# Kernel tuning notes

Measured on AMD Instinct MI355X. Metric: run time of the kernel, lower is better.

Reference implementation:

```python
import jax, jax.numpy as jnp
import numpy as np

N_PROP = 1024; C_FEAT = 32
ROI = 7; SR = 6; S = ROI * SR
NMS_THR = 0.01; NMS_K = 100
X_MIN, Z_MAX, VOX = -40.0, 70.0, 0.1

_SIGNS = np.array([[sx, sy, sz] for sx in (-1, 1) for sy in (-1, 1) for sz in (-1, 1)], np.float32)


def project_to_bev(a):
    # anchors [N,6] = (x,y,z,dx,dy,dz); BEV pixel box (x right, z forward->down)
    x, z, dx, dz = a[:, 0], a[:, 2], a[:, 3], a[:, 5]
    return jnp.stack([(x - dx * 0.5 - X_MIN) / VOX,
                      (Z_MAX - (z + dz * 0.5)) / VOX,
                      (x + dx * 0.5 - X_MIN) / VOX,
                      (Z_MAX - (z - dz * 0.5)) / VOX], axis=1)


def project_to_img(a, P, image_shape):
    # axis-aligned 3D box -> 8 corners -> project with P [3,4] -> min/max, clip
    corners = a[:, None, :3] + _SIGNS[None] * (a[:, None, 3:6] * 0.5)  # [N,8,3]
    hom = jnp.concatenate([corners, jnp.ones_like(corners[..., :1])], -1)
    proj = jnp.einsum('nkj,ij->nki', hom, P)
    z = jnp.maximum(proj[..., 2], 0.1)
    u, v = proj[..., 0] / z, proj[..., 1] / z
    H = image_shape[0].astype(u.dtype); W = image_shape[1].astype(u.dtype)
    return jnp.stack([jnp.clip(u.min(1), 0., W), jnp.clip(v.min(1), 0., H),
                      jnp.clip(u.max(1), 0., W), jnp.clip(v.max(1), 0., H)], 1)


def roi_align(feat, boxes):
    # feat [C,H,W], boxes [N,4] xyxy; aligned=True, sampling_ratio=SR, scale=1.0
    C, H, W = feat.shape
    grid = (jnp.arange(S, dtype=feat.dtype) + 0.5) / S

    def one(box):
        x1, y1, x2, y2 = box[0] - 0.5, box[1] - 0.5, box[2] - 0.5, box[3] - 0.5
        xs = x1 + grid * (x2 - x1)
        ys = y1 + grid * (y2 - y1)
        x0 = jnp.clip(jnp.floor(xs), 0, W - 1); y0 = jnp.clip(jnp.floor(ys), 0, H - 1)
        wx = jnp.clip(xs - x0, 0., 1.); wy = jnp.clip(ys - y0, 0., 1.)
        x0i = x0.astype(jnp.int32); y0i = y0.astype(jnp.int32)
        x1i = jnp.minimum(x0i + 1, W - 1); y1i = jnp.minimum(y0i + 1, H - 1)
        g = lambda yi, xi: feat[:, yi[:, None], xi[None, :]]  # [C,S,S]
        val = (g(y0i, x0i) * ((1 - wy)[:, None] * (1 - wx)[None, :])
             + g(y0i, x1i) * ((1 - wy)[:, None] * wx[None, :])
             + g(y1i, x0i) * (wy[:, None] * (1 - wx)[None, :])
             + g(y1i, x1i) * (wy[:, None] * wx[None, :]))
        return val.reshape(C, ROI, SR, ROI, SR).mean(axis=(2, 4))

    return jax.vmap(one)(boxes)  # [N,C,7,7]


def nms(boxes, scores, thr, k):
    areas = (boxes[:, 2] - boxes[:, 0]) * (boxes[:, 3] - boxes[:, 1])

    def step(s, _):
        i = jnp.argmax(s)
        b = boxes[i]
        xx1 = jnp.maximum(boxes[:, 0], b[0]); yy1 = jnp.maximum(boxes[:, 1], b[1])
        xx2 = jnp.minimum(boxes[:, 2], b[2]); yy2 = jnp.minimum(boxes[:, 3], b[3])
        inter = jnp.maximum(xx2 - xx1, 0.) * jnp.maximum(yy2 - yy1, 0.)
        iou = inter / (areas + areas[i] - inter + 1e-6)
        s = jnp.where(iou > thr, -jnp.inf, s).at[i].set(-jnp.inf)
        return s, i

    _, idx = jax.lax.scan(step, scores, None, length=k)
    return idx


def setup_inputs() -> dict:
    key = jax.random.key(0)
    ks = jax.random.split(key, 8)
    u = jax.random.uniform(ks[0], (N_PROP, 6))
    x = u[:, 0] * 70. - 35.; y = u[:, 1] * 2. - 1.; z = u[:, 2] * 60. + 5.
    dims = u[:, 3:6] * 3. + 1.
    top_anchors = jnp.concatenate([jnp.stack([x, y, z], 1), dims], 1)
    f = 721.5377
    calib = jnp.array([[f, 0., 609.56, 44.857],
                       [0., f, 172.854, 0.2163],
                       [0., 0., 1., 0.00275]], jnp.float32)
    D = C_FEAT * ROI * ROI
    w = lambda k, shp: jax.random.normal(k, shp, jnp.float32) * 0.02
    return {
        'img_feat_map': jax.random.normal(ks[1], (1, C_FEAT, 360, 1200), jnp.float32),
        'bev_feat_map': jax.random.normal(ks[2], (1, C_FEAT, 700, 800), jnp.float32),
        'top_anchors': top_anchors, 'calib': calib,
        'ground_plane': jnp.array([0., -1., 0., 1.65], jnp.float32),
        'img_mask': jnp.ones((1, 1, 1, 1), jnp.float32),
        'bev_mask': jnp.ones((1, 1, 1, 1), jnp.float32),
        'W1': w(ks[3], (D, 2048)), 'b1': jnp.zeros((2048,), jnp.float32),
        'W2': w(ks[4], (2048, 2048)), 'b2': jnp.zeros((2048,), jnp.float32),
        'Wc': w(ks[5], (2048, 2)), 'bc': jnp.zeros((2,), jnp.float32),
        'Wo': w(ks[6], (2048, 10)), 'bo': jnp.zeros((10,), jnp.float32),
        'Wa': w(ks[7], (2048, 2)), 'ba': jnp.zeros((2,), jnp.float32),
        'image_shape': jnp.array([360, 1200], jnp.int32),
    }


def reference(img_feat_map, bev_feat_map, top_anchors, calib, ground_plane,
              img_mask, bev_mask, W1, b1, W2, b2, Wc, bc, Wo, bo, Wa, ba, image_shape):
    bev_boxes = project_to_bev(top_anchors)
    img_boxes = project_to_img(top_anchors, calib, image_shape)
    rois_rgb = roi_align((img_mask * img_feat_map)[0], img_boxes)
    rois_bev = roi_align((bev_mask * bev_feat_map)[0], bev_boxes)
    fused = (rois_rgb + rois_bev) / (img_mask + bev_mask)[0, 0, 0, 0]  # mean fusion
    h = fused.reshape(fused.shape[0], -1)
    h = jax.nn.relu(h @ W1 + b1)
    h = jax.nn.relu(h @ W2 + b2)
    obj = h @ Wc + bc    # [N,2]
    off = h @ Wo + bo    # [N,10]
    ang = h @ Wa + ba    # [N,2]
    obj_soft = jax.nn.softmax(obj, axis=1)
    orient = jnp.arctan2(ang[:, 1], ang[:, 0])
    pred_anchors = top_anchors + off[:, :6] + 0.0 * ground_plane.sum()
    pred_box = jnp.concatenate([pred_anchors, jnp.zeros_like(pred_anchors[:, :1])], 1)
    pred_bev = project_to_bev(pred_anchors)
    top_scores = obj[:, 1:].max(axis=1)  # max over fg classes
    idx = nms(pred_bev, top_scores, NMS_THR, NMS_K)
    return (obj_soft[idx], pred_anchors[idx], off[idx], pred_box[idx], orient[idx])
```

## Files before the change

### kernel.cpp

```cpp
#include <hip/hip_runtime.h>
#include <math.h>

#define N_PROP 1024
#define C_FEAT 32
#define ROI 7
#define SR 6
#define S_GRID 42
#define IMG_H 360
#define IMG_W 1200
#define BEV_H 700
#define BEV_W 800
#define D_FEAT (C_FEAT*ROI*ROI)
#define HID 2048
#define NMS_K 100
#define NMS_THR 0.01f

typedef __attribute__((ext_vector_type(8))) short bf16x8;
typedef __attribute__((ext_vector_type(4))) float f32x4;
typedef __attribute__((ext_vector_type(2), aligned(4))) float f32x2u;
typedef __attribute__((ext_vector_type(4), aligned(4))) float f32x4u;

#define WS_IMG_BOXES 0
#define WS_BEV_BOXES (WS_IMG_BOXES + 4*N_PROP)
#define WS_OBJS      (WS_BEV_BOXES + 4*N_PROP)
#define WS_OFF       (WS_OBJS + 2*N_PROP)
#define WS_ORIENT    (WS_OFF + 10*N_PROP)
#define WS_PRED      (WS_ORIENT + N_PROP)
#define WS_PBEV      (WS_PRED + 6*N_PROP)
#define WS_SCORES    (WS_PBEV + 4*N_PROP)
#define WS_IDX       (WS_SCORES + N_PROP)
#define WS_SORT      (WS_IDX + 128)
#define WS_R0        40960
#define WS_R1        (WS_R0 + N_PROP*D_FEAT)
#define WS_IMGT      WS_R1
#define WS_FUSED_HI  (WS_R0 + 2*N_PROP*D_FEAT)
#define WS_FUSED_LO  (WS_FUSED_HI + N_PROP*D_FEAT/2)
#define WS_H1HI      WS_R0
#define WS_H1LO      (WS_R0 + N_PROP*HID/2)
#define WS_H2        (WS_R0 + N_PROP*HID)
#define WS_NMSM      WS_R0

__device__ __forceinline__ unsigned int bf16_rtn(float x) {
    unsigned int u = __float_as_uint(x);
    return (u + 0x7FFFu + ((u >> 16) & 1u)) >> 16;
}

__global__ void boxes_kernel(const float* __restrict__ anchors,
                             const float* __restrict__ calib,
                             const int* __restrict__ imshape,
                             float* __restrict__ img_boxes,
                             float* __restrict__ bev_boxes) {
    int n = blockIdx.x * blockDim.x + threadIdx.x;
    if (n >= N_PROP) return;
    float x = anchors[n*6+0], y = anchors[n*6+1], z = anchors[n*6+2];
    float dx = anchors[n*6+3], dy = anchors[n*6+4], dz = anchors[n*6+5];

    bev_boxes[n*4+0] = ((x - dx*0.5f) - (-40.0f)) / 0.1f;
    bev_boxes[n*4+1] = (70.0f - (z + dz*0.5f)) / 0.1f;
    bev_boxes[n*4+2] = ((x + dx*0.5f) - (-40.0f)) / 0.1f;
    bev_boxes[n*4+3] = (70.0f - (z - dz*0.5f)) / 0.1f;

    float P[12];
    #pragma unroll
    for (int i = 0; i < 12; i++) P[i] = calib[i];

    float umin = 1e30f, vmin = 1e30f, umax = -1e30f, vmax = -1e30f;
    #pragma unroll
    for (int k = 0; k < 8; k++) {
        float fsx = (k & 4) ? 1.0f : -1.0f;
        float fsy = (k & 2) ? 1.0f : -1.0f;
        float fsz = (k & 1) ? 1.0f : -1.0f;
        float cx = x + fsx * dx * 0.5f;
        float cy = y + fsy * dy * 0.5f;
        float cz = z + fsz * dz * 0.5f;
        float p0 = P[0]*cx + P[1]*cy + P[2]*cz + P[3];
        float p1 = P[4]*cx + P[5]*cy + P[6]*cz + P[7];
        float p2 = P[8]*cx + P[9]*cy + P[10]*cz + P[11];
        float zz = fmaxf(p2, 0.1f);
        float u = p0 / zz, v = p1 / zz;
        umin = fminf(umin, u); umax = fmaxf(umax, u);
        vmin = fminf(vmin, v); vmax = fmaxf(vmax, v);
    }
    float Hf = (float)imshape[0];
    float Wf = (float)imshape[1];
    img_boxes[n*4+0] = fminf(fmaxf(umin, 0.0f), Wf);
    img_boxes[n*4+1] = fminf(fmaxf(vmin, 0.0f), Hf);
    img_boxes[n*4+2] = fminf(fmaxf(umax, 0.0f), Wf);
    img_boxes[n*4+3] = fminf(fmaxf(vmax, 0.0f), Hf);
}

__global__ __launch_bounds__(256) void transpose_img_kernel(
        const float* __restrict__ in, float* __restrict__ out, int c0) {
    __shared__ float lds[64*9];
    int y = blockIdx.y;
    int x0 = blockIdx.x * 64;
    int xl = threadIdx.x & 63;
    int ch = threadIdx.x >> 6;
    int x = x0 + xl;
    #pragma unroll
    for (int i = 0; i < 2; i++) {
        int c = ch + i*4;
        float v = 0.0f;
        if (x < IMG_W)
            v = in[(size_t)(c0+c)*IMG_H*IMG_W + (size_t)y*IMG_W + x];
        lds[xl*9 + c] = v;
    }
    __syncthreads();
    int c8 = threadIdx.x & 7;
    int xp = threadIdx.x >> 3;
    #pragma unroll
    for (int j = 0; j < 2; j++) {
        int xx = x0 + xp + j*32;
        if (xx < IMG_W)
            out[((size_t)y*IMG_W + xx)*8 + c8] = lds[(xp + j*32)*9 + c8];
    }
}

__global__ __launch_bounds__(256) void roi_img_cl_kernel(
        const float* __restrict__ T, const float* __restrict__ img_boxes,
        float* __restrict__ img_out, int c0) {
    int b = blockIdx.x;
    __shared__ float s_xw[S_GRID], s_yw[S_GRID];
    __shared__ int   s_xi[S_GRID], s_yr[S_GRID];
    __shared__ float s_out[8*49];
    int tid = threadIdx.x;
    if (tid < S_GRID) {
        float g = ((float)tid + 0.5f) / (float)S_GRID;
        float bx1 = img_boxes[b*4+0] - 0.5f, by1 = img_boxes[b*4+1] - 0.5f;
        float bx2 = img_boxes[b*4+2] - 0.5f, by2 = img_boxes[b*4+3] - 0.5f;
        float xs = bx1 + g * (bx2 - bx1);
        float x0f = fminf(fmaxf(floorf(xs), 0.0f), (float)(IMG_W-2));
        s_xw[tid] = fminf(fmaxf(xs - x0f, 0.0f), 1.0f);
        s_xi[tid] = (int)x0f * 8;
        float ys = by1 + g * (by2 - by1);
        float y0f = fminf(fmaxf(floorf(ys), 0.0f), (float)(IMG_H-2));
        s_yw[tid] = fminf(fmaxf(ys - y0f, 0.0f), 1.0f);
        s_yr[tid] = (int)y0f * (IMG_W*8);
    }
    __syncthreads();

    int wv   = tid >> 6;
    int lane = tid & 63;
    int sy2 = lane >> 5;
    int sxb = (lane >> 4) & 1;
    int px  = (lane >> 1) & 7;
    int c4  = lane & 1;
    bool act = (px < 7);

    for (int pyi = 0; pyi < 2; pyi++) {
        int py = wv + pyi*4;
        if (py > 6) break;
        f32x4 acc = {0.f, 0.f, 0.f, 0.f};
        if (act) {
            #pragma unroll
            for (int t = 0; t < 3; t++) {
                int sy = py*6 + t*2 + sy2;
                int row0 = s_yr[sy];
                float wy = s_yw[sy];
                #pragma unroll
                for (int s = 0; s < 3; s++) {
                    int sx = px*6 + s*2 + sxb;
                    int col = s_xi[sx] + c4*4;
                    const float* p00 = T + row0 + col;
                    f32x4 v00 = *(const f32x4*)(p00);
                    f32x4 v01 = *(const f32x4*)(p00 + 8);
                    f32x4 v10 = *(const f32x4*)(p00 + IMG_W*8);
                    f32x4 v11 = *(const f32x4*)(p00 + IMG_W*8 + 8);
                    float wx = s_xw[sx];
                    #pragma unroll
                    for (int e = 0; e < 4; e++) {
                        float top = fmaf(wx, v01[e] - v00[e], v00[e]);
                        float bot = fmaf(wx, v11[e] - v10[e], v10[e]);
                        acc[e] += fmaf(wy, bot - top, top);
                    }
                }
            }
        }
        #pragma unroll
        for (int e = 0; e < 4; e++) acc[e] += __shfl_xor(acc[e], 32);
        #pragma unroll
        for (int e = 0; e < 4; e++) acc[e] += __shfl_xor(acc[e], 16);
        if (act && sy2 == 0 && sxb == 0) {
            #pragma unroll
            for (int e = 0; e < 4; e++)
                s_out[(c4*4+e)*49 + py*7 + px] = acc[e];
        }
    }
    __syncthreads();
    float* op = img_out + (size_t)b * D_FEAT + c0*49;
    for (int t = tid; t < 8*49; t += 256) op[t] = s_out[t];
}

__global__ __launch_bounds__(64, 8) void roi_bev_kernel(
        const float* __restrict__ bevF, const float* __restrict__ bev_boxes,
        float* __restrict__ bev_out) {
    int gx = blockIdx.x;
    int b  = blockIdx.y;
    int c0 = gx * 3;
    int nch = (C_FEAT - c0 < 3) ? (C_FEAT - c0) : 3;
    const int W = BEV_W, H = BEV_H;

    int lane = threadIdx.x;
    __shared__ int   s_xi[S_GRID];
    __shared__ float s_xw[S_GRID];
    __shared__ int   s_row0[S_GRID];
    __shared__ float s_wy[S_GRID];

    if (lane < S_GRID) {
        float g = ((float)lane + 0.5f) / (float)S_GRID;
        float bx1 = bev_boxes[b*4+0], by1 = bev_boxes[b*4+1];
        float bx2 = bev_boxes[b*4+2], by2 = bev_boxes[b*4+3];
        float e1 = bx1 - 0.5f, e2 = bx2 - 0.5f;
        float xs = e1 + g * (e2 - e1);
        float x0f = fminf(fmaxf(floorf(xs), 0.0f), (float)(W-2));
        s_xw[lane] = fminf(fmaxf(xs - x0f, 0.0f), 1.0f);
        s_xi[lane] = (int)x0f;
        float d1 = by1 - 0.5f, d2 = by2 - 0.5f;
        float ys = d1 + g * (d2 - d1);
        float y0f = fminf(fmaxf(floorf(ys), 0.0f), (float)(H-2));
        s_wy[lane] = fminf(fmaxf(ys - y0f, 0.0f), 1.0f);
        s_row0[lane] = (int)y0f * W;
    }
    __syncthreads();

    int gl = lane / 21;
    int j  = lane - gl*21;
    bool act = (gl < nch);

    int basecol = 0;
    float wa0=0.f,wa1=0.f,wa2=0.f,wa3=0.f;
    float wb0=0.f,wb1=0.f,wb2=0.f,wb3=0.f;
    if (act) {
        int x0a = s_xi[2*j];
        int x0b = s_xi[2*j+1];
        float wxa = s_xw[2*j], wxb = s_xw[2*j+1];
        basecol = min(x0a, W-4);
        int ca = x0a - basecol;
        int cb = min(x0b - basecol, 2);
        wa0 = (ca==0)? 1.f-wxa : 0.f;
        wa1 = (ca==0)? wxa : ((ca==1)? 1.f-wxa : 0.f);
        wa2 = (ca==1)? wxa : ((ca==2)? 1.f-wxa : 0.f);
        wa3 = (ca==2)? wxa : 0.f;
        wb0 = (cb==0)? 1.f-wxb : 0.f;
        wb1 = (cb==0)? wxb : ((cb==1)? 1.f-wxb : 0.f);
        wb2 = (cb==1)? wxb : ((cb==2)? 1.f-wxb : 0.f);
        wb3 = (cb==2)? wxb : 0.f;
    }
    const float* fp = bevF + (size_t)(c0 + (act ? gl : 0)) * W * H + basecol;
    int pxw = j / 3;
    bool wr = act && (j - pxw*3 == 0);
    float* op = bev_out + (size_t)b * D_FEAT + (c0+gl)*49;

    #pragma unroll 1
    for (int py = 0; py < ROI; py++) {
        float pl = 0.0f;
        #pragma unroll
        for (int sy = 0; sy < SR; sy++) {
            int yi = py*SR + sy;
            int r0 = s_row0[yi];
            float wy = s_wy[yi];
            if (act) {
                f32x4u q0 = *(const f32x4u*)(fp + r0);
                f32x4u q1 = *(const f32x4u*)(fp + r0 + W);
                float tA = fmaf(q0.x,wa0, fmaf(q0.y,wa1, fmaf(q0.z,wa2, q0.w*wa3)));
                float bA = fmaf(q1.x,wa0, fmaf(q1.y,wa1, fmaf(q1.z,wa2, q1.w*wa3)));
                float tB = fmaf(q0.x,wb0, fmaf(q0.y,wb1, fmaf(q0.z,wb2, q0.w*wb3)));
                float bB = fmaf(q1.x,wb0, fmaf(q1.y,wb1, fmaf(q1.z,wb2, q1.w*wb3)));
                pl += fmaf(wy, bA - tA, tA);
                pl += fmaf(wy, bB - tB, tB);
            }
        }
        float s = pl + __shfl_down(pl, 1) + __shfl_down(pl, 2);
        if (wr) op[py*ROI + pxw] = s;
    }
}

__global__ __launch_bounds__(256) void combine_split_kernel(
        const float4* __restrict__ img, const float4* __restrict__ bev,
        const float* __restrict__ img_mask, const float* __restrict__ bev_mask,
        ushort4* __restrict__ outHi, ushort4* __restrict__ outLo, int total4) {
    int i = blockIdx.x * 256 + threadIdx.x;
    if (i >= total4) return;
    float m0 = img_mask[0], m1 = bev_mask[0];
    float inv = 1.0f / ((m0 + m1) * 36.0f);
    float w0 = m0 * inv, w1 = m1 * inv;
    float4 a = img[i], b = bev[i];
    float v[4] = { w0*a.x + w1*b.x, w0*a.y + w1*b.y, w0*a.z + w1*b.z, w0*a.w + w1*b.w };
    ushort4 hv, lv;
    unsigned short* hp = &hv.x;
    unsigned short* lp = &lv.x;
    #pragma unroll
    for (int e = 0; e < 4; e++) {
        unsigned int rh = bf16_rtn(v[e]);
        float lo = v[e] - __uint_as_float(rh << 16);
        hp[e] = (unsigned short)rh;
        lp[e] = (unsigned short)bf16_rtn(lo);
    }
    outHi[i] = hv;
    outLo[i] = lv;
}

#define LDK 40
template<int EPI>
__global__ __launch_bounds__(256) void gemm_bf16x2_kernel(
        const unsigned short* __restrict__ Ahi, const unsigned short* __restrict__ Alo,
        const float* __restrict__ W, const float* __restrict__ bias, int K,
        unsigned short* __restrict__ outHi, unsigned short* __restrict__ outLo,
        float* __restrict__ outF) {
    __shared__ short AsH[64*LDK], AsL[64*LDK];
    __shared__ short BsH[128*LDK], BsL[128*LDK];

    const int tid = threadIdx.x;
    const int m0 = blockIdx.y * 64, n0 = blockIdx.x * 128;

    const int am = tid >> 2, ac = tid & 3;
    const uint4* ApH = (const uint4*)(Ahi + (size_t)(m0 + am) * K + ac*8);
    const uint4* ApL = (const uint4*)(Alo + (size_t)(m0 + am) * K + ac*8);
    const int nn = tid & 127, rbase = (tid >> 7) * 16;
    const float* Bp = W + (size_t)rbase * 2048 + n0 + nn;

    const int lane = tid & 63, wave = tid >> 6;
    const int wm = wave & 1, wn = wave >> 1;
    const int l15 = lane & 15, quad = lane >> 4;

    f32x4 acc[2][4];
    #pragma unroll
    for (int i = 0; i < 2; i++)
        #pragma unroll
        for (int j = 0; j < 4; j++)
            acc[i][j] = (f32x4){0.f, 0.f, 0.f, 0.f};

    const int nK = K >> 5;
    uint4 aHr = ApH[0];
    uint4 aLr = ApL[0];
    float bReg[16];
    #pragma unroll
    for (int j = 0; j < 16; j++) bReg[j] = Bp[(size_t)j * 2048];

    for (int ks = 0; ks < nK; ks++) {
        __syncthreads();
        *(uint4*)&AsH[am*LDK + ac*8] = aHr;
        *(uint4*)&AsL[am*LDK + ac*8] = aLr;
        {
            unsigned short hv[16], lv[16];
            #pragma unroll
            for (int j = 0; j < 16; j++) {
                unsigned int rh = bf16_rtn(bReg[j]);
                float lo = bReg[j] - __uint_as_float(rh << 16);
                hv[j] = (unsigned short)rh;
                lv[j] = (unsigned short)bf16_rtn(lo);
            }
            *(uint4*)&BsH[nn*LDK + rbase + 0] = *(uint4*)&hv[0];
            *(uint4*)&BsH[nn*LDK + rbase + 8] = *(uint4*)&hv[8];
            *(uint4*)&BsL[nn*LDK + rbase + 0] = *(uint4*)&lv[0];
            *(uint4*)&BsL[nn*LDK + rbase + 8] = *(uint4*)&lv[8];
        }
        __syncthreads();
        if (ks + 1 < nK) {
            int k0n = (ks + 1) * 32;
            aHr = ApH[k0n >> 3];
            aLr = ApL[k0n >> 3];
            #pragma unroll
            for (int j = 0; j < 16; j++) bReg[j] = Bp[(size_t)(k0n + j) * 2048];
        }
        const short* aBH = AsH + (wm*32 + l15)*LDK + quad*8;
        const short* aBL = AsL + (wm*32 + l15)*LDK + quad*8;
        const short* bBH = BsH + (wn*64 + l15)*LDK + quad*8;
        const short* bBL = BsL + (wn*64 + l15)*LDK + quad*8;
        bf16x8 aH0 = *(const bf16x8*)(aBH);
        bf16x8 aH1 = *(const bf16x8*)(aBH + 16*LDK);
        bf16x8 aL0 = *(const bf16x8*)(aBL);
        bf16x8 aL1 = *(const bf16x8*)(aBL + 16*LDK);
        #pragma unroll
        for (int nt = 0; nt < 4; nt++) {
            bf16x8 bH = *(const bf16x8*)(bBH + nt*16*LDK);
            bf16x8 bL = *(const bf16x8*)(bBL + nt*16*LDK);
            acc[0][nt] = __builtin_amdgcn_mfma_f32_16x16x32_bf16(aH0, bH, acc[0][nt], 0, 0, 0);
            acc[0][nt] = __builtin_amdgcn_mfma_f32_16x16x32_bf16(aH0, bL, acc[0][nt], 0, 0, 0);
            acc[0][nt] = __builtin_amdgcn_mfma_f32_16x16x32_bf16(aL0, bH, acc[0][nt], 0, 0, 0);
            acc[1][nt] = __builtin_amdgcn_mfma_f32_16x16x32_bf16(aH1, bH, acc[1][nt], 0, 0, 0);
            acc[1][nt] = __builtin_amdgcn_mfma_f32_16x16x32_bf16(aH1, bL, acc[1][nt], 0, 0, 0);
            acc[1][nt] = __builtin_amdgcn_mfma_f32_16x16x32_bf16(aL1, bH, acc[1][nt], 0, 0, 0);
        }
    }

    #pragma unroll
    for (int mt = 0; mt < 2; mt++) {
        #pragma unroll
        for (int nt = 0; nt < 4; nt++) {
            int n = n0 + wn*64 + nt*16 + l15;
            float bv = bias[n];
            #pragma unroll
            for (int reg = 0; reg < 4; reg++) {
                int m = m0 + wm*32 + mt*16 + quad*4 + reg;
                float v = fmaxf(acc[mt][nt][reg] + bv, 0.0f);
                if (EPI == 1) {
                    unsigned int rh = bf16_rtn(v);
                    float lo = v - __uint_as_float(rh << 16);
                    outHi[(size_t)m * 2048 + n] = (unsigned short)rh;
                    outLo[(size_t)m * 2048 + n] = (unsigned short)bf16_rtn(lo);
                } else {
                    outF[(size_t)m * 2048 + n] = v;
                }
            }
        }
    }
}

__global__ __launch_bounds__(256) void heads_kernel(
        const float* __restrict__ h,
        const float* __restrict__ Wc, const float* __restrict__ bc,
        const float* __restrict__ Wo, const float* __restrict__ bo,
        const float* __restrict__ Wa, const float* __restrict__ ba,
        const float* __restrict__ anchors,
        float* __restrict__ obj_soft, float* __restrict__ off_out,
        float* __restrict__ orient, float* __restrict__ pred,
        float* __restrict__ pbev, float* __restrict__ scores) {
    int row = blockIdx.x;
    const float* hr = h + (size_t)row * HID;
    float acc[14];
    #pragma unroll
    for (int j = 0; j < 14; j++) acc[j] = 0.0f;
    for (int k = threadIdx.x; k < HID; k += 256) {
        float hv = hr[k];
        acc[0]  += hv * Wc[k*2+0];
        acc[1]  += hv * Wc[k*2+1];
        #pragma unroll
        for (int j = 0; j < 10; j++) acc[2+j] += hv * Wo[k*10+j];
        acc[12] += hv * Wa[k*2+0];
        acc[13] += hv * Wa[k*2+1];
    }
    #pragma unroll
    for (int d = 32; d > 0; d >>= 1) {
        #pragma unroll
        for (int j = 0; j < 14; j++) acc[j] += __shfl_down(acc[j], d);
    }
    __shared__ float red[4][14];
    int wid = threadIdx.x >> 6, lane = threadIdx.x & 63;
    if (lane == 0) {
        #pragma unroll
        for (int j = 0; j < 14; j++) red[wid][j] = acc[j];
    }
    __syncthreads();
    if (threadIdx.x == 0) {
        float f[14];
        #pragma unroll
        for (int j = 0; j < 14; j++)
            f[j] = red[0][j] + red[1][j] + red[2][j] + red[3][j];
        float obj0 = f[0] + bc[0], obj1 = f[1] + bc[1];
        float offv[10];
        #pragma unroll
        for (int j = 0; j < 10; j++) offv[j] = f[2+j] + bo[j];
        float ang0 = f[12] + ba[0], ang1 = f[13] + ba[1];
        float mx = fmaxf(obj0, obj1);
        float e0 = expf(obj0 - mx), e1 = expf(obj1 - mx);
        float den = e0 + e1;
        obj_soft[row*2+0] = e0 / den;
        obj_soft[row*2+1] = e1 / den;
        scores[row] = obj1;
        orient[row] = atan2f(ang1, ang0);
        float pa[6];
        #pragma unroll
        for (int j = 0; j < 6; j++) {
            pa[j] = anchors[row*6+j] + offv[j];
            pred[row*6+j] = pa[j];
        }
        #pragma unroll
        for (int j = 0; j < 10; j++) off_out[row*10+j] = offv[j];
        float x = pa[0], z = pa[2], ddx = pa[3], ddz = pa[5];
        pbev[row*4+0] = ((x - ddx*0.5f) - (-40.0f)) / 0.1f;
        pbev[row*4+1] = (70.0f - (z + ddz*0.5f)) / 0.1f;
        pbev[row*4+2] = ((x + ddx*0.5f) - (-40.0f)) / 0.1f;
        pbev[row*4+3] = (70.0f - (z - ddz*0.5f)) / 0.1f;
    }
}

__global__ __launch_bounds__(256) void nms_mask_kernel(
        const float* __restrict__ boxes, unsigned long long* __restrict__ M) {
    int i = blockIdx.x;
    const float4* bp = (const float4*)boxes;
    float4 bi4 = bp[i];
    float ai = (bi4.z - bi4.x) * (bi4.w - bi4.y);
    int lane = threadIdx.x & 63, wave = threadIdx.x >> 6;
    #pragma unroll
    for (int it = 0; it < 4; it++) {
        int q = it*256 + wave*64 + lane;
        float4 bq = bp[q];
        float aq = (bq.z - bq.x) * (bq.w - bq.y);
        float xx1 = fmaxf(bi4.x, bq.x), yy1 = fmaxf(bi4.y, bq.y);
        float xx2 = fminf(bi4.z, bq.z), yy2 = fminf(bi4.w, bq.w);
        float inter = fmaxf(xx2 - xx1, 0.0f) * fmaxf(yy2 - yy1, 0.0f);
        float iou = inter / (ai + aq - inter + 1e-6f);
        unsigned long long bal = __ballot(iou > NMS_THR);
        if (lane == 0) M[(size_t)i*16 + it*4 + wave] = bal;
    }
}

__global__ __launch_bounds__(256) void nms_rank_kernel(
        const float* __restrict__ scores, int* __restrict__ sorted) {
    int i = blockIdx.x;
    unsigned int u = __float_as_uint(scores[i]);
    unsigned int ki = (u & 0x80000000u) ? ~u : (u | 0x80000000u);
    unsigned long long keyi = ((unsigned long long)ki << 10) | (unsigned)(1023 - i);
    int cnt = 0;
    #pragma unroll
    for (int t = 0; t < 4; t++) {
        int j = threadIdx.x + t*256;
        unsigned int uj = __float_as_uint(scores[j]);
        unsigned int kj = (uj & 0x80000000u) ? ~uj : (uj | 0x80000000u);
        unsigned long long keyj = ((unsigned long long)kj << 10) | (unsigned)(1023 - j);
        cnt += (keyj > keyi) ? 1 : 0;
    }
    #pragma unroll
    for (int d = 32; d > 0; d >>= 1) cnt += __shfl_down(cnt, d);
    __shared__ int red[4];
    if ((threadIdx.x & 63) == 0) red[threadIdx.x >> 6] = cnt;
    __syncthreads();
    if (threadIdx.x == 0) sorted[red[0] + red[1] + red[2] + red[3]] = i;
}

__global__ void nms_scan2_kernel(const int* __restrict__ sorted,
                                 const unsigned long long* __restrict__ M,
                                 int* __restrict__ idx_out) {
    int lane = threadIdx.x;
    unsigned long long sup = 0ull;
    int n = 0;
    for (int chunk = 0; chunk < 16 && n < NMS_K; chunk++) {
        int cid = sorted[chunk*64 + lane];
        int cw = cid >> 6, cb = cid & 63;
        unsigned long long supw = __shfl(sup, cw);
        unsigned long long mask = __ballot(((supw >> cb) & 1ull) == 0ull);
        while (mask != 0ull && n < NMS_K) {
            int p = __ffsll(mask) - 1;
            int c = __shfl(cid, p);
            if (lane == 0) idx_out[n] = c;
            n++;
            unsigned long long roww = (lane < 16) ? M[(size_t)c*16 + lane] : 0ull;
            sup |= roww;
            unsigned long long tw = __shfl(roww, cw);
            unsigned long long kill = __ballot(((tw >> cb) & 1ull) != 0ull);
            mask &= ~kill;
            mask &= ~(1ull << p);
        }
    }
    if (lane == 0) {
        for (; n < NMS_K; n++) idx_out[n] = 0;
    }
}

__global__ void gather_kernel(const int* __restrict__ idx,
                              const float* __restrict__ obj_soft,
                              const float* __restrict__ pred,
                              const float* __restrict__ off,
                              const float* __restrict__ orient,
                              float* __restrict__ out) {
    int i = threadIdx.x;
    if (i < NMS_K) {
        int j = idx[i];
        out[2*i+0] = obj_soft[j*2+0];
        out[2*i+1] = obj_soft[j*2+1];
        #pragma unroll
        for (int t = 0; t < 6; t++) out[200 + 6*i + t] = pred[j*6+t];
        #pragma unroll
        for (int t = 0; t < 10; t++) out[800 + 10*i + t] = off[j*10+t];
        #pragma unroll
        for (int t = 0; t < 6; t++) out[1800 + 7*i + t] = pred[j*6+t];
        out[1800 + 7*i + 6] = 0.0f;
        out[2500 + i] = orient[j];
    }
}

extern "C" void kernel_launch(void* const* d_in, const int* in_sizes, int n_in,
                              void* d_out, int out_size, void* d_ws, size_t ws_size,
                              hipStream_t stream) {
    const float* imgF     = (const float*)d_in[0];
    const float* bevF     = (const float*)d_in[1];
    const float* anchors  = (const float*)d_in[2];
    const float* calib    = (const float*)d_in[3];
    const float* img_mask = (const float*)d_in[5];
    const float* bev_mask = (const float*)d_in[6];
    const float* W1 = (const float*)d_in[7];
    const float* b1 = (const float*)d_in[8];
    const float* W2 = (const float*)d_in[9];
    const float* b2 = (const float*)d_in[10];
    const float* Wc = (const float*)d_in[11];
    const float* bc = (const float*)d_in[12];
    const float* Wo = (const float*)d_in[13];
    const float* bo = (const float*)d_in[14];
    const float* Wa = (const float*)d_in[15];
    const float* ba = (const float*)d_in[16];
    const int* image_shape = (const int*)d_in[17];

    float* ws = (float*)d_ws;
    float* img_boxes = ws + WS_IMG_BOXES;
    float* bev_boxes = ws + WS_BEV_BOXES;
    float* obj_soft  = ws + WS_OBJS;
    float* off       = ws + WS_OFF;
    float* orient    = ws + WS_ORIENT;
    float* pred      = ws + WS_PRED;
    float* pbev      = ws + WS_PBEV;
    float* scores    = ws + WS_SCORES;
    int*   idx       = (int*)(ws + WS_IDX);
    int*   sorted    = (int*)(ws + WS_SORT);
    float* img_s     = ws + WS_R0;
    float* bev_s     = ws + WS_R1;
    float* img_t     = ws + WS_IMGT;
    unsigned short* fusedHi = (unsigned short*)(ws + WS_FUSED_HI);
    unsigned short* fusedLo = (unsigned short*)(ws + WS_FUSED_LO);
    unsigned short* h1Hi    = (unsigned short*)(ws + WS_H1HI);
    unsigned short* h1Lo    = (unsigned short*)(ws + WS_H1LO);
    float* h2        = ws + WS_H2;
    unsigned long long* nmsM = (unsigned long long*)(ws + WS_NMSM);

    boxes_kernel<<<N_PROP/64, 64, 0, stream>>>(anchors, calib, image_shape,
                                               img_boxes, bev_boxes);
    for (int ch = 0; ch < 4; ch++) {
        transpose_img_kernel<<<dim3((IMG_W+63)/64, IMG_H), 256, 0, stream>>>(
            imgF, img_t, ch*8);
        roi_img_cl_kernel<<<N_PROP, 256, 0, stream>>>(
            img_t, img_boxes, img_s, ch*8);
    }
    roi_bev_kernel<<<dim3(11, N_PROP), 64, 0, stream>>>(
        bevF, bev_boxes, bev_s);
    combine_split_kernel<<<(N_PROP*D_FEAT/4 + 255)/256, 256, 0, stream>>>(
        (const float4*)img_s, (const float4*)bev_s, img_mask, bev_mask,
        (ushort4*)fusedHi, (ushort4*)fusedLo, N_PROP*D_FEAT/4);
    gemm_bf16x2_kernel<1><<<dim3(16, 16), 256, 0, stream>>>(
        fusedHi, fusedLo, W1, b1, D_FEAT, h1Hi, h1Lo, nullptr);
    gemm_bf16x2_kernel<0><<<dim3(16, 16), 256, 0, stream>>>(
        h1Hi, h1Lo, W2, b2, HID, nullptr, nullptr, h2);
    heads_kernel<<<N_PROP, 256, 0, stream>>>(h2, Wc, bc, Wo, bo, Wa, ba, anchors,
                                             obj_soft, off, orient, pred, pbev, scores);
    nms_mask_kernel<<<N_PROP, 256, 0, stream>>>(pbev, nmsM);
    nms_rank_kernel<<<N_PROP, 256, 0, stream>>>(scores, sorted);
    nms_scan2_kernel<<<1, 64, 0, stream>>>(sorted, nmsM, idx);
    gather_kernel<<<1, 128, 0, stream>>>(idx, obj_soft, pred, off, orient,
                                         (float*)d_out);
}
```

Measured before the change: 560.1 us.

## Double-buffer LDS tiles in split-bf16 GEMM to cut barriers per K step

Converts the GEMM main loop to ping-pong shared-memory buffers with two register prefetch stages. The next tile's LDS store and bf16 split overlap the MFMA compute on the current buffer, and only one barrier is needed per K step instead of two. In exchange, LDS use doubles and register pressure rises from two sets of prefetch registers, which may lower occupancy.

```diff
diff --git a/kernel.cpp b/kernel.cpp
--- a/kernel.cpp
+++ b/kernel.cpp
@@ -301,14 +301,57 @@
 }
 
 #define LDK 40
+#define GLOAD(ks, S) { \
+    int k0_ = (ks) * 32; \
+    aH##S = ApH[k0_ >> 3]; \
+    aL##S = ApL[k0_ >> 3]; \
+    _Pragma("unroll") \
+    for (int j_ = 0; j_ < 16; j_++) bR##S[j_] = Bp[(size_t)(k0_ + j_) * 2048]; }
+
+#define LSTORE(S, B) { \
+    *(uint4*)&AsH[B][am*LDK + ac*8] = aH##S; \
+    *(uint4*)&AsL[B][am*LDK + ac*8] = aL##S; \
+    unsigned short hv_[16], lv_[16]; \
+    _Pragma("unroll") \
+    for (int j_ = 0; j_ < 16; j_++) { \
+        unsigned int rh_ = bf16_rtn(bR##S[j_]); \
+        float lo_ = bR##S[j_] - __uint_as_float(rh_ << 16); \
+        hv_[j_] = (unsigned short)rh_; \
+        lv_[j_] = (unsigned short)bf16_rtn(lo_); } \
+    *(uint4*)&BsH[B][nn*LDK + rbase + 0] = *(uint4*)&hv_[0]; \
+    *(uint4*)&BsH[B][nn*LDK + rbase + 8] = *(uint4*)&hv_[8]; \
+    *(uint4*)&BsL[B][nn*LDK + rbase + 0] = *(uint4*)&lv_[0]; \
+    *(uint4*)&BsL[B][nn*LDK + rbase + 8] = *(uint4*)&lv_[8]; }
+
+#define KCOMPUTE(B) { \
+    const short* aBH = &AsH[B][(wm*32 + l15)*LDK + quad*8]; \
+    const short* aBL = &AsL[B][(wm*32 + l15)*LDK + quad*8]; \
+    const short* bBH = &BsH[B][(wn*64 + l15)*LDK + quad*8]; \
+    const short* bBL = &BsL[B][(wn*64 + l15)*LDK + quad*8]; \
+    bf16x8 aH0 = *(const bf16x8*)(aBH); \
+    bf16x8 aH1 = *(const bf16x8*)(aBH + 16*LDK); \
+    bf16x8 aL0 = *(const bf16x8*)(aBL); \
+    bf16x8 aL1 = *(const bf16x8*)(aBL + 16*LDK); \
+    _Pragma("unroll") \
+    for (int nt = 0; nt < 4; nt++) { \
+        bf16x8 bH = *(const bf16x8*)(bBH + nt*16*LDK); \
+        bf16x8 bL = *(const bf16x8*)(bBL + nt*16*LDK); \
+        acc[0][nt] = __builtin_amdgcn_mfma_f32_16x16x32_bf16(aH0, bH, acc[0][nt], 0, 0, 0); \
+        acc[0][nt] = __builtin_amdgcn_mfma_f32_16x16x32_bf16(aH0, bL, acc[0][nt], 0, 0, 0); \
+        acc[0][nt] = __builtin_amdgcn_mfma_f32_16x16x32_bf16(aL0, bH, acc[0][nt], 0, 0, 0); \
+        acc[1][nt] = __builtin_amdgcn_mfma_f32_16x16x32_bf16(aH1, bH, acc[1][nt], 0, 0, 0); \
+        acc[1][nt] = __builtin_amdgcn_mfma_f32_16x16x32_bf16(aH1, bL, acc[1][nt], 0, 0, 0); \
+        acc[1][nt] = __builtin_amdgcn_mfma_f32_16x16x32_bf16(aL1, bH, acc[1][nt], 0, 0, 0); \
+    } }
+
 template<int EPI>
 __global__ __launch_bounds__(256) void gemm_bf16x2_kernel(
         const unsigned short* __restrict__ Ahi, const unsigned short* __restrict__ Alo,
         const float* __restrict__ W, const float* __restrict__ bias, int K,
         unsigned short* __restrict__ outHi, unsigned short* __restrict__ outLo,
         float* __restrict__ outF) {
-    __shared__ short AsH[64*LDK], AsL[64*LDK];
-    __shared__ short BsH[128*LDK], BsL[128*LDK];
+    __shared__ short AsH[2][64*LDK], AsL[2][64*LDK];
+    __shared__ short BsH[2][128*LDK], BsL[2][128*LDK];
 
     const int tid = threadIdx.x;
     const int m0 = blockIdx.y * 64, n0 = blockIdx.x * 128;
@@ -331,57 +374,27 @@
             acc[i][j] = (f32x4){0.f, 0.f, 0.f, 0.f};
 
     const int nK = K >> 5;
-    uint4 aHr = ApH[0];
-    uint4 aLr = ApL[0];
-    float bReg[16];
-    #pragma unroll
-    for (int j = 0; j < 16; j++) bReg[j] = Bp[(size_t)j * 2048];
-
-    for (int ks = 0; ks < nK; ks++) {
+    uint4 aHA, aLA, aHB, aLB;
+    float bRA[16], bRB[16];
+
+    GLOAD(0, A);
+    LSTORE(A, 0);
+    GLOAD(1, B);
+
+    int ks = 0;
+    while (true) {
         __syncthreads();
-        *(uint4*)&AsH[am*LDK + ac*8] = aHr;
-        *(uint4*)&AsL[am*LDK + ac*8] = aLr;
-        {
-            unsigned short hv[16], lv[16];
-            #pragma unroll
-            for (int j = 0; j < 16; j++) {
-                unsigned int rh = bf16_rtn(bReg[j]);
-                float lo = bReg[j] - __uint_as_float(rh << 16);
-                hv[j] = (unsigned short)rh;
-                lv[j] = (unsigned short)bf16_rtn(lo);
-            }
-            *(uint4*)&BsH[nn*LDK + rbase + 0] = *(uint4*)&hv[0];
-            *(uint4*)&BsH[nn*LDK + rbase + 8] = *(uint4*)&hv[8];
-            *(uint4*)&BsL[nn*LDK + rbase + 0] = *(uint4*)&lv[0];
-            *(uint4*)&BsL[nn*LDK + rbase + 8] = *(uint4*)&lv[8];
-        }
+        if (ks + 1 < nK) LSTORE(B, 1);
+        if (ks + 2 < nK) GLOAD(ks + 2, A);
+        KCOMPUTE(0);
+        ks++;
+        if (ks >= nK) break;
         __syncthreads();
-        if (ks + 1 < nK) {
-            int k0n = (ks + 1) * 32;
-            aHr = ApH[k0n >> 3];
-            aLr = ApL[k0n >> 3];
-            #pragma unroll
-            for (int j = 0; j < 16; j++) bReg[j] = Bp[(size_t)(k0n + j) * 2048];
-        }
-        const short* aBH = AsH + (wm*32 + l15)*LDK + quad*8;
-        const short* aBL = AsL + (wm*32 + l15)*LDK + quad*8;
-        const short* bBH = BsH + (wn*64 + l15)*LDK + quad*8;
-        const short* bBL = BsL + (wn*64 + l15)*LDK + quad*8;
-        bf16x8 aH0 = *(const bf16x8*)(aBH);
-        bf16x8 aH1 = *(const bf16x8*)(aBH + 16*LDK);
-        bf16x8 aL0 = *(const bf16x8*)(aBL);
-        bf16x8 aL1 = *(const bf16x8*)(aBL + 16*LDK);
-        #pragma unroll
-        for (int nt = 0; nt < 4; nt++) {
-            bf16x8 bH = *(const bf16x8*)(bBH + nt*16*LDK);
-            bf16x8 bL = *(const bf16x8*)(bBL + nt*16*LDK);
-            acc[0][nt] = __builtin_amdgcn_mfma_f32_16x16x32_bf16(aH0, bH, acc[0][nt], 0, 0, 0);
-            acc[0][nt] = __builtin_amdgcn_mfma_f32_16x16x32_bf16(aH0, bL, acc[0][nt], 0, 0, 0);
-            acc[0][nt] = __builtin_amdgcn_mfma_f32_16x16x32_bf16(aL0, bH, acc[0][nt], 0, 0, 0);
-            acc[1][nt] = __builtin_amdgcn_mfma_f32_16x16x32_bf16(aH1, bH, acc[1][nt], 0, 0, 0);
-            acc[1][nt] = __builtin_amdgcn_mfma_f32_16x16x32_bf16(aH1, bL, acc[1][nt], 0, 0, 0);
-            acc[1][nt] = __builtin_amdgcn_mfma_f32_16x16x32_bf16(aL1, bH, acc[1][nt], 0, 0, 0);
-        }
+        if (ks + 1 < nK) LSTORE(A, 0);
+        if (ks + 2 < nK) GLOAD(ks + 2, B);
+        KCOMPUTE(1);
+        ks++;
+        if (ks >= nK) break;
     }
 
     #pragma unroll
```

New measurement: 528.2 us. -5.7%, faster.
